# Kernel optimization log

Measured on AMD Instinct MI355X. Metric: run time of the kernel, lower is better.

Reference implementation:

```python
import jax, jax.numpy as jnp
import numpy as np

N, E, F, H, G, C = 50000, 800000, 128, 128, 500, 10
L = 3  # num_conv_layers
EPS = 1e-5


def batch_norm(x, g, b):
    # training-mode BatchNorm1d: biased variance, eps=1e-5
    mu = jnp.mean(x, axis=0)
    var = jnp.var(x, axis=0)
    return (x - mu) * jax.lax.rsqrt(var + EPS) * g + b


def gcn_conv(x, W, bias, src, dst, n):
    # x' = D^{-1/2} (A + I) D^{-1/2} (x W) + bias, edge weights = 1
    xw = x @ W
    loop = jnp.arange(n)
    s = jnp.concatenate([src, loop])  # sources incl. self-loops
    d = jnp.concatenate([dst, loop])  # targets incl. self-loops
    w = jnp.ones(s.shape[0], x.dtype)
    deg = jax.ops.segment_sum(w, s, num_segments=n)
    dinv = jnp.where(deg > 0, jax.lax.rsqrt(deg), 0.0)
    norm = dinv[s] * w * dinv[d]
    msg = xw[s] * norm[:, None]  # gather + scale
    out = jax.ops.segment_sum(msg, d, num_segments=n)  # scatter-add
    return out + bias


def setup_inputs() -> dict:
    key = jax.random.key(0)
    ks = jax.random.split(key, 16)
    x = jax.random.normal(ks[0], (N, F), dtype=jnp.float32)
    edge_index = jax.random.randint(ks[1], (2, E), 0, N, dtype=jnp.int64)
    batch = jnp.sort(jax.random.randint(ks[2], (N,), 0, G, dtype=jnp.int64))
    sF = 1.0 / np.sqrt(F)
    sH = 1.0 / np.sqrt(H)
    return {
        "x": x,
        "edge_index": edge_index,
        "batch": batch,
        "bn_feat_g": jnp.ones((F,), jnp.float32),
        "bn_feat_b": jnp.full((F,), 1e-4, jnp.float32),
        "W_feat": jax.random.normal(ks[3], (F, H), jnp.float32) * sF,
        "bns_conv_g": jnp.ones((L, H), jnp.float32),
        "bns_conv_b": jnp.full((L, H), 1e-4, jnp.float32),
        "W_conv": jax.random.normal(ks[4], (L, H, H), jnp.float32) * sH,
        "b_conv": jnp.zeros((L, H), jnp.float32),
        "bn_fc_g": jnp.ones((H,), jnp.float32),
        "bn_fc_b": jnp.full((H,), 1e-4, jnp.float32),
        "W_lin": jax.random.normal(ks[5], (H, H), jnp.float32) * sH,
        "b_lin": jnp.zeros((H,), jnp.float32),
        "bn_hid_g": jnp.ones((H,), jnp.float32),
        "bn_hid_b": jnp.full((H,), 1e-4, jnp.float32),
        "W_cls": jax.random.normal(ks[6], (H, C), jnp.float32) * sH,
        "b_cls": jnp.zeros((C,), jnp.float32),
    }


def reference(x, edge_index, batch, bn_feat_g, bn_feat_b, W_feat,
              bns_conv_g, bns_conv_b, W_conv, b_conv,
              bn_fc_g, bn_fc_b, W_lin, b_lin,
              bn_hid_g, bn_hid_b, W_cls, b_cls):
    src, dst = edge_index[0], edge_index[1]
    h = batch_norm(x, bn_feat_g, bn_feat_b)
    h = jax.nn.relu(h @ W_feat)  # gfn conv: linear only, no bias/propagation
    for i in range(L):
        h = batch_norm(h, bns_conv_g[i], bns_conv_b[i])
        h = jax.nn.relu(gcn_conv(h, W_conv[i], b_conv[i], src, dst, N))
    h = jax.ops.segment_sum(h, batch, num_segments=G)  # global_add_pool
    h = batch_norm(h, bn_fc_g, bn_fc_b)
    h = jax.nn.relu(h @ W_lin + b_lin)
    h = batch_norm(h, bn_hid_g, bn_hid_b)
    logits = h @ W_cls + b_cls
    return jax.nn.log_softmax(logits, axis=-1)
```

## Files before the change

### kernel.cpp

```cpp
#include <hip/hip_runtime.h>

#define NF 128
#define EPS 1e-5f
#define KELL 64
#define NPART 8
#define KP 16
#define HB 64
#define HRANGE 32768

typedef unsigned short ushort_t;
typedef unsigned int uint_t;

using bf16x8 = __attribute__((ext_vector_type(8))) short;
using f32x4  = __attribute__((ext_vector_type(4))) float;
using f32x2  = __attribute__((ext_vector_type(2))) float;

static __device__ inline ushort_t f2bf(float f) {
    uint_t u = __float_as_uint(f);
    return (ushort_t)((u + 0x7fffu + ((u >> 16) & 1u)) >> 16);
}


__global__ void k_fill_ell(const int* __restrict__ ei, int* __restrict__ dcnt8,
                           ushort_t* __restrict__ colx8, int E, int n) {
    int e = blockIdx.x * 256 + threadIdx.x;
    int p = blockIdx.x & (NPART - 1);
    if (e < E) {
        int s = ei[e], d = ei[E + e];
        int pos = atomicAdd(&dcnt8[p * n + d], 1);
        if (pos < KP) colx8[((size_t)p * n + d) * KP + pos] = (ushort_t)s;
    }
}

__global__ void k_hist(const int* __restrict__ ei, uint_t* __restrict__ partial, int E) {
    __shared__ uint_t h2[HRANGE / 2];
    int b = blockIdx.x, t = threadIdx.x;
#pragma unroll
    for (int p = 0; p < 2; ++p) {
        int base = p * HRANGE;
        for (int w = t; w < HRANGE / 2; w += 256) h2[w] = 0;
        __syncthreads();
        for (int e = b * 256 + t; e < E; e += HB * 256) {
            unsigned u = (unsigned)(ei[e] - base);
            if (u < HRANGE)
                atomicAdd(&h2[u >> 1], 1u << ((u & 1) << 4));
        }
        __syncthreads();
        uint_t* dst = partial + ((size_t)(p * HB + b) << 14);
        for (int w = t; w < HRANGE / 2; w += 256) dst[w] = h2[w];
        __syncthreads();
    }
}

__global__ void k_finish(const int* __restrict__ dcnt8, const uint_t* __restrict__ partial,
                         int* __restrict__ ucnt, float* __restrict__ dinv,
                         const ushort_t* __restrict__ colx8, ushort_t* __restrict__ colx,
                         ushort_t* __restrict__ BbSent, int n) {
    int i = blockIdx.x * 256 + threadIdx.x;
    if (i < n) {
        {
            int p = i >> 15;
            int u = i & (HRANGE - 1);
            int w = u >> 1, sh = (u & 1) << 4;
            const uint_t* base = partial + ((size_t)(p * HB) << 14) + w;
            uint_t sum = 0;
#pragma unroll 8
            for (int b = 0; b < HB; ++b) sum += base[(size_t)b << 14];
            sum = (sum >> sh) & 0xffffu;
            dinv[i] = rsqrtf((float)sum + 1.0f);
        }
        ushort_t* row = colx + (size_t)i * KELL;
        int w = 0;
#pragma unroll
        for (int p = 0; p < NPART; ++p) {
            int c = dcnt8[p * n + i];
            if (c > KP) c = KP;
            const ushort_t* src = colx8 + ((size_t)p * n + i) * KP;
            for (int j = 0; j < c && w < KELL - 1; ++j) row[w++] = src[j];
        }
        ucnt[i] = w;
        row[w] = (ushort_t)i;
        int len = (w + 16) & ~15;
        for (int q = w + 1; q < len; ++q) row[q] = (ushort_t)n;
    }
    if (blockIdx.x == 0 && threadIdx.x < 64)
        ((uint_t*)BbSent)[threadIdx.x] = 0;
}


__global__ void bn_stats(const float* __restrict__ h, float* __restrict__ stats, int n) {
    int j = threadIdx.x & 127;
    int half = threadIdx.x >> 7;
    float s = 0.f, q = 0.f;
    for (int r = blockIdx.x * 2 + half; r < n; r += gridDim.x * 2) {
        float v = h[r * NF + j];
        s += v;
        q += v * v;
    }
    __shared__ float ls[256], lq[256];
    ls[threadIdx.x] = s; lq[threadIdx.x] = q;
    __syncthreads();
    if (threadIdx.x < 128) {
        atomicAdd(&stats[j], ls[threadIdx.x] + ls[threadIdx.x + 128]);
        atomicAdd(&stats[NF + j], lq[threadIdx.x] + lq[threadIdx.x + 128]);
    }
}


__global__ void pack_w4(const float* __restrict__ W0, const float* __restrict__ W123,
                        ushort_t* __restrict__ Wp) {
    int gidx = blockIdx.x * 256 + threadIdx.x;
    int mat = gidx >> 11, idx = gidx & 2047;
    const float* W = (mat == 0) ? W0 : (W123 + (size_t)(mat - 1) * NF * NF);
    int lane = idx & 63, ct = (idx >> 6) & 7, kc = idx >> 9;
    int m = lane & 15, q = lane >> 4;
    ushort_t o[8];
#pragma unroll
    for (int j = 0; j < 8; ++j)
        o[j] = f2bf(W[(kc * 32 + q * 8 + j) * NF + ct * 16 + m]);
    *(uint4*)&Wp[(size_t)gidx * 8] = *(uint4*)o;
}


#define HSTRIDE 136

__launch_bounds__(256)
__global__ void gemm_mfma(const float* __restrict__ Hh, const ushort_t* __restrict__ Wp,
                          const float* __restrict__ stats, const float* __restrict__ gW,
                          const float* __restrict__ bB, float inv_n,
                          const float* __restrict__ bias, const float* __restrict__ rowscale,
                          float* __restrict__ out, ushort_t* __restrict__ outb,
                          int nrows, int relu, int obf) {
    __shared__ ushort_t hs[64 * HSTRIDE];
    __shared__ float acs[256];
    const int tid = threadIdx.x;
    const int rb = blockIdx.x * 64;

    if (tid < 128) {
        float mean = stats[tid] * inv_n;
        float var = stats[NF + tid] * inv_n - mean * mean;
        float rstd = rsqrtf(var + EPS);
        float a = gW[tid] * rstd;
        acs[tid] = a;
        acs[NF + tid] = bB[tid] - mean * a;
    }
    __syncthreads();
    const float4* ac4 = (const float4*)acs;

#pragma unroll
    for (int p = 0; p < 8; ++p) {
        int idx = p * 256 + tid;
        int r = idx >> 5, k4 = idx & 31;
        int gr = rb + r;
        float4 v = (gr < nrows) ? *(const float4*)&Hh[(size_t)gr * NF + k4 * 4]
                                : make_float4(0.f, 0.f, 0.f, 0.f);
        float4 a4 = ac4[k4], c4 = ac4[32 + k4];
        ushort_t o[4];
        o[0] = f2bf(fmaf(v.x, a4.x, c4.x));
        o[1] = f2bf(fmaf(v.y, a4.y, c4.y));
        o[2] = f2bf(fmaf(v.z, a4.z, c4.z));
        o[3] = f2bf(fmaf(v.w, a4.w, c4.w));
        *(uint2*)&hs[r * HSTRIDE + k4 * 4] = *(uint2*)o;
    }
    __syncthreads();

    const int wave = tid >> 6, lane = tid & 63;
    const int m = lane & 15, q = lane >> 4;
    const ushort_t* arow = &hs[(wave * 16 + m) * HSTRIDE];

    f32x4 acc[8];
#pragma unroll
    for (int ct = 0; ct < 8; ++ct) acc[ct] = (f32x4){0.f, 0.f, 0.f, 0.f};

#pragma unroll
    for (int kc = 0; kc < 4; ++kc) {
        bf16x8 af = *(const bf16x8*)&arow[kc * 32 + q * 8];
        const ushort_t* wp = Wp + kc * 4096 + lane * 8;
#pragma unroll
        for (int ct = 0; ct < 8; ++ct) {
            bf16x8 bfr = *(const bf16x8*)&wp[ct * 512];
            acc[ct] = __builtin_amdgcn_mfma_f32_16x16x32_bf16(af, bfr, acc[ct], 0, 0, 0);
        }
    }

#pragma unroll
    for (int r = 0; r < 4; ++r) {
        int grow = rb + wave * 16 + q * 4 + r;
        if (grow < nrows) {
            float rs = (obf && rowscale) ? rowscale[grow] : 1.0f;
#pragma unroll
            for (int ct = 0; ct < 8; ++ct) {
                int col = ct * 16 + m;
                float v = acc[ct][r] + (bias ? bias[col] : 0.f);
                if (relu) v = fmaxf(v, 0.f);
                if (obf) outb[(size_t)grow * NF + col] = f2bf(v * rs);
                else     out[(size_t)grow * NF + col] = v;
            }
        }
    }
}


__launch_bounds__(256)
__global__ void gemm_bn(const float* __restrict__ Hh, const float* __restrict__ W,
                        const float* __restrict__ stats, const float* __restrict__ gW,
                        const float* __restrict__ bB, float inv_n,
                        const float* __restrict__ bias,
                        float* __restrict__ out, int nrows, int relu) {
    __shared__ float hsb[64][133];
    __shared__ float acs[256];
    const int tid = threadIdx.x;
    const int tx = tid & 15;
    const int ty = tid >> 4;
    const int rb = blockIdx.x * 64;

    if (tid < 128) {
        float mean = stats[tid] * inv_n;
        float var = stats[NF + tid] * inv_n - mean * mean;
        float rstd = rsqrtf(var + EPS);
        float a = gW[tid] * rstd;
        acs[tid] = a;
        acs[NF + tid] = bB[tid] - mean * a;
    }
    __syncthreads();

#pragma unroll 8
    for (int p = 0; p < 32; ++p) {
        int idx = p * 256 + tid;
        int r = idx >> 7, k = idx & 127;
        int gr = rb + r;
        float v = (gr < nrows) ? Hh[(size_t)gr * NF + k] : 0.f;
        hsb[r][k] = fmaf(v, acs[k], acs[NF + k]);
    }
    __syncthreads();

    float acc[4][8];
#pragma unroll
    for (int i = 0; i < 4; ++i)
#pragma unroll
        for (int j = 0; j < 8; ++j) acc[i][j] = 0.f;

    const int c0 = tx * 4, c1 = 64 + tx * 4;
#pragma unroll 4
    for (int k = 0; k < 128; ++k) {
        const float4 b0 = *(const float4*)&W[k * NF + c0];
        const float4 b1 = *(const float4*)&W[k * NF + c1];
#pragma unroll
        for (int i = 0; i < 4; ++i) {
            float a = hsb[ty * 4 + i][k];
            acc[i][0] = fmaf(a, b0.x, acc[i][0]);
            acc[i][1] = fmaf(a, b0.y, acc[i][1]);
            acc[i][2] = fmaf(a, b0.z, acc[i][2]);
            acc[i][3] = fmaf(a, b0.w, acc[i][3]);
            acc[i][4] = fmaf(a, b1.x, acc[i][4]);
            acc[i][5] = fmaf(a, b1.y, acc[i][5]);
            acc[i][6] = fmaf(a, b1.z, acc[i][6]);
            acc[i][7] = fmaf(a, b1.w, acc[i][7]);
        }
    }

#pragma unroll
    for (int i = 0; i < 4; ++i) {
        int gr = rb + ty * 4 + i;
        if (gr < nrows) {
            float o[8];
#pragma unroll
            for (int j = 0; j < 8; ++j) {
                int c = (j < 4) ? (c0 + j) : (c1 + j - 4);
                float v = acc[i][j] + (bias ? bias[c] : 0.f);
                o[j] = relu ? fmaxf(v, 0.f) : v;
            }
            *(float4*)&out[(size_t)gr * NF + c0] = make_float4(o[0], o[1], o[2], o[3]);
            *(float4*)&out[(size_t)gr * NF + c1] = make_float4(o[4], o[5], o[6], o[7]);
        }
    }
}


#define ACC2(u, j) { f32x2 t;                                   \
    t.x = __uint_as_float((u) << 16);                           \
    t.y = __uint_as_float((u) & 0xffff0000u);                   \
    acc2[j] += t; }
#define ACC8(q) { ACC2(q.x, 0) ACC2(q.y, 1) ACC2(q.z, 2) ACC2(q.w, 3) }

__launch_bounds__(256)
__global__ void k_aggregate_bf(const ushort_t* __restrict__ xwb, const int* __restrict__ ucnt,
                               const ushort_t* __restrict__ colx, const float* __restrict__ dinv,
                               const float* __restrict__ bias, float* __restrict__ out, int n) {
    int node = blockIdx.x * 16 + (threadIdx.x >> 4);
    int lane = threadIdx.x & 15;
    if (node >= n) return;
    const uint4* __restrict__ xq = (const uint4*)xwb;
    f32x2 acc2[4];
#pragma unroll
    for (int j = 0; j < 4; ++j) acc2[j] = (f32x2){0.f, 0.f};
    int dc = min(ucnt[node], KELL - 1);
    int len = (dc + 16) & ~15;
    int e0 = node * KELL;
    for (int e = e0; e < e0 + len; e += 16) {
        uint4 ia = *(const uint4*)&colx[e];
        uint4 ib = *(const uint4*)&colx[e + 8];
        int i0 = ia.x & 0xffff, i1 = ia.x >> 16;
        int i2 = ia.y & 0xffff, i3 = ia.y >> 16;
        int i4 = ia.z & 0xffff, i5 = ia.z >> 16;
        int i6 = ia.w & 0xffff, i7 = ia.w >> 16;
        int i8 = ib.x & 0xffff, i9 = ib.x >> 16;
        int iA = ib.y & 0xffff, iB = ib.y >> 16;
        int iC = ib.z & 0xffff, iD = ib.z >> 16;
        int iE = ib.w & 0xffff, iF = ib.w >> 16;
        uint4 q0 = xq[(size_t)i0 * 16 + lane];
        uint4 q1 = xq[(size_t)i1 * 16 + lane];
        uint4 q2 = xq[(size_t)i2 * 16 + lane];
        uint4 q3 = xq[(size_t)i3 * 16 + lane];
        uint4 q4 = xq[(size_t)i4 * 16 + lane];
        uint4 q5 = xq[(size_t)i5 * 16 + lane];
        uint4 q6 = xq[(size_t)i6 * 16 + lane];
        uint4 q7 = xq[(size_t)i7 * 16 + lane];
        uint4 q8 = xq[(size_t)i8 * 16 + lane];
        uint4 q9 = xq[(size_t)i9 * 16 + lane];
        uint4 qA = xq[(size_t)iA * 16 + lane];
        uint4 qB = xq[(size_t)iB * 16 + lane];
        uint4 qC = xq[(size_t)iC * 16 + lane];
        uint4 qD = xq[(size_t)iD * 16 + lane];
        uint4 qE = xq[(size_t)iE * 16 + lane];
        uint4 qF = xq[(size_t)iF * 16 + lane];
        ACC8(q0) ACC8(q1) ACC8(q2) ACC8(q3)
        ACC8(q4) ACC8(q5) ACC8(q6) ACC8(q7)
        ACC8(q8) ACC8(q9) ACC8(qA) ACC8(qB)
        ACC8(qC) ACC8(qD) ACC8(qE) ACC8(qF)
    }
    float di = dinv[node];
    float4 b0 = *(const float4*)&bias[lane * 8];
    float4 b1 = *(const float4*)&bias[lane * 8 + 4];
    float4 o0, o1;
    o0.x = fmaxf(fmaf(di, acc2[0].x, b0.x), 0.f);
    o0.y = fmaxf(fmaf(di, acc2[0].y, b0.y), 0.f);
    o0.z = fmaxf(fmaf(di, acc2[1].x, b0.z), 0.f);
    o0.w = fmaxf(fmaf(di, acc2[1].y, b0.w), 0.f);
    o1.x = fmaxf(fmaf(di, acc2[2].x, b1.x), 0.f);
    o1.y = fmaxf(fmaf(di, acc2[2].y, b1.y), 0.f);
    o1.z = fmaxf(fmaf(di, acc2[3].x, b1.z), 0.f);
    o1.w = fmaxf(fmaf(di, acc2[3].y, b1.w), 0.f);
    *(float4*)&out[(size_t)node * NF + lane * 8] = o0;
    *(float4*)&out[(size_t)node * NF + lane * 8 + 4] = o1;
}


__global__ void k_pool(const float* __restrict__ h, const int* __restrict__ batch,
                       float* __restrict__ pooled, float* __restrict__ stats, int n) {
    int g = blockIdx.x;
    int t = threadIdx.x;
    int lo = 0, hi = n;
    while (lo < hi) { int m = (lo + hi) >> 1; if (batch[m] < g) lo = m + 1; else hi = m; }
    int start = lo;
    lo = start; hi = n;
    while (lo < hi) { int m = (lo + hi) >> 1; if (batch[m] < g + 1) lo = m + 1; else hi = m; }
    int end = lo;
    float a0 = 0.f, a1 = 0.f, a2 = 0.f, a3 = 0.f;
    int r = start;
    for (; r + 4 <= end; r += 4) {
        a0 += h[(size_t)r * NF + t];
        a1 += h[(size_t)(r + 1) * NF + t];
        a2 += h[(size_t)(r + 2) * NF + t];
        a3 += h[(size_t)(r + 3) * NF + t];
    }
    for (; r < end; ++r) a0 += h[(size_t)r * NF + t];
    float val = (a0 + a1) + (a2 + a3);
    pooled[g * NF + t] = val;
    atomicAdd(&stats[t], val);
    atomicAdd(&stats[NF + t], val * val);
}


__global__ void k_cls(const float* __restrict__ h, const float* __restrict__ stats,
                      const float* __restrict__ gW, const float* __restrict__ bB,
                      float inv_n, const float* __restrict__ Wc,
                      const float* __restrict__ bc, float* __restrict__ out, int C_) {
    __shared__ float hr[128];
    __shared__ float lg[16];
    __shared__ float lse_s;
    int r = blockIdx.x, t = threadIdx.x;
#pragma unroll
    for (int half = 0; half < 2; ++half) {
        int j = t + half * 64;
        float mean = stats[j] * inv_n;
        float var = stats[NF + j] * inv_n - mean * mean;
        float rstd = rsqrtf(var + EPS);
        float a = gW[j] * rstd;
        float c = bB[j] - mean * a;
        hr[j] = fmaf(h[r * NF + j], a, c);
    }
    __syncthreads();
    if (t < C_) {
        float s = bc[t];
        for (int k = 0; k < 128; ++k) s = fmaf(hr[k], Wc[k * C_ + t], s);
        lg[t] = s;
    }
    __syncthreads();
    if (t == 0) {
        float m = -1e30f;
        for (int c = 0; c < C_; ++c) m = fmaxf(m, lg[c]);
        float se = 0.f;
        for (int c = 0; c < C_; ++c) se += expf(lg[c] - m);
        lse_s = m + logf(se);
    }
    __syncthreads();
    if (t < C_) out[r * C_ + t] = lg[t] - lse_s;
}


extern "C" void kernel_launch(void* const* d_in, const int* in_sizes, int n_in,
                              void* d_out, int out_size, void* d_ws, size_t ws_size,
                              hipStream_t stream) {
    const float* x          = (const float*)d_in[0];
    const int*   ei         = (const int*)d_in[1];
    const int*   batch      = (const int*)d_in[2];
    const float* bn_feat_g  = (const float*)d_in[3];
    const float* bn_feat_b  = (const float*)d_in[4];
    const float* W_feat     = (const float*)d_in[5];
    const float* bns_conv_g = (const float*)d_in[6];
    const float* bns_conv_b = (const float*)d_in[7];
    const float* W_conv     = (const float*)d_in[8];
    const float* b_conv     = (const float*)d_in[9];
    const float* bn_fc_g    = (const float*)d_in[10];
    const float* bn_fc_b    = (const float*)d_in[11];
    const float* W_lin      = (const float*)d_in[12];
    const float* b_lin      = (const float*)d_in[13];
    const float* bn_hid_g   = (const float*)d_in[14];
    const float* bn_hid_b   = (const float*)d_in[15];
    const float* W_cls      = (const float*)d_in[16];
    const float* b_cls      = (const float*)d_in[17];
    float* outp = (float*)d_out;

    const int N_ = in_sizes[2];
    const int E_ = in_sizes[1] / 2;
    const int C_ = 10;
    const int G_ = out_size / C_;

    char* wsp = (char*)d_ws;
    auto alloc = [&](size_t bytes) {
        void* p = (void*)wsp;
        wsp += (bytes + 255) & ~(size_t)255;
        return p;
    };
    int*      dcnt8  = (int*)alloc((size_t)NPART * N_ * 4);
    float*    statsA = (float*)alloc(6 * 256 * 4);
    float*    A      = (float*)alloc((size_t)N_ * NF * 4);
    ushort_t* Bb     = (ushort_t*)alloc((size_t)(N_ + 1) * NF * 2);
    float*    dinv   = (float*)alloc((size_t)N_ * 4);
    int*      ucnt   = (int*)alloc((size_t)N_ * 4);
    ushort_t* colx8  = (ushort_t*)alloc((size_t)NPART * N_ * KP * 2);
    ushort_t* colx   = (ushort_t*)alloc((size_t)N_ * KELL * 2);
    uint_t*   hpart  = (uint_t*)alloc((size_t)2 * HB * (HRANGE / 2) * 4);
    ushort_t* Wp     = (ushort_t*)alloc((size_t)4 * NF * NF * 2);
    float*    pooled = (float*)alloc((size_t)G_ * NF * 4);
    float*    y2     = (float*)alloc((size_t)G_ * NF * 4);

    float* st_x  = statsA;
    float* st_f  = statsA + 256;
    float* st_a1 = statsA + 512;
    float* st_a2 = statsA + 768;
    float* st_pl = statsA + 1024;
    float* st_y2 = statsA + 1280;

    int nb_n = (N_ + 255) / 256;
    int nb_e = (E_ + 255) / 256;
    int nb_g = (N_ + 63) / 64;

    size_t cnt_rounded = (((size_t)NPART * N_ * 4) + 255) & ~(size_t)255;
    hipMemsetAsync(dcnt8, 0, cnt_rounded + 6 * 256 * 4, stream);

    k_fill_ell<<<nb_e, 256, 0, stream>>>(ei, dcnt8, colx8, E_, N_);
    k_hist<<<HB, 256, 0, stream>>>(ei, hpart, E_);
    k_finish<<<nb_n, 256, 0, stream>>>(dcnt8, hpart, ucnt, dinv, colx8, colx,
                                       Bb + (size_t)N_ * NF, N_);

    pack_w4<<<32, 256, 0, stream>>>(W_feat, W_conv, Wp);

    bn_stats<<<512, 256, 0, stream>>>(x, st_x, N_);
    gemm_mfma<<<nb_g, 256, 0, stream>>>(x, Wp, st_x, bn_feat_g, bn_feat_b, 1.0f / N_,
                                        nullptr, nullptr, A, nullptr, N_, 1, 0);
    bn_stats<<<512, 256, 0, stream>>>(A, st_f, N_);

    float* st_in[3] = {st_f, st_a1, st_a2};
    float* st_out[3] = {st_a1, st_a2, nullptr};
    for (int l = 0; l < 3; ++l) {
        gemm_mfma<<<nb_g, 256, 0, stream>>>(A, Wp + (size_t)(l + 1) * NF * NF,
                                            st_in[l], bns_conv_g + l * NF, bns_conv_b + l * NF,
                                            1.0f / N_, nullptr, dinv, nullptr, Bb, N_, 0, 1);
        k_aggregate_bf<<<(N_ + 15) / 16, 256, 0, stream>>>(Bb, ucnt, colx, dinv,
                                                           b_conv + l * NF, A, N_);
        if (st_out[l])
            bn_stats<<<512, 256, 0, stream>>>(A, st_out[l], N_);
    }

    k_pool<<<G_, 128, 0, stream>>>(A, batch, pooled, st_pl, N_);

    gemm_bn<<<(G_ + 63) / 64, 256, 0, stream>>>(pooled, W_lin, st_pl, bn_fc_g, bn_fc_b,
                                                1.0f / G_, b_lin, y2, G_, 1);
    bn_stats<<<512, 256, 0, stream>>>(y2, st_y2, G_);

    k_cls<<<G_, 64, 0, stream>>>(y2, st_y2, bn_hid_g, bn_hid_b, 1.0f / G_,
                                 W_cls, b_cls, outp, C_);
}
```

Baseline: 503.4 us.

## Build ELL adjacency via two-level bucketing by destination block in LDS

Replaces the per-partition global atomic ELL fill and its later merge with a bucket pass: edges are binned by destination block of 256 nodes using shared-memory counts plus one global atomic per bucket. A second kernel then builds each block's ELL rows in LDS and writes them out coalesced. This removes the large 8-partition count array, its memset and the scattered global atomics. The cost is a fixed bucket capacity (BCAP), so overflow edges are dropped, and a hard limit of 256 buckets, i.e. at most 65536 nodes. The order of neighbours within a row becomes nondeterministic.

```diff
diff --git a/kernel.cpp b/kernel.cpp
--- a/kernel.cpp
+++ b/kernel.cpp
@@ -3,10 +3,9 @@
 #define NF 128
 #define EPS 1e-5f
 #define KELL 64
-#define NPART 8
-#define KP 16
 #define HB 64
 #define HRANGE 32768
+#define BCAP 5120
 
 typedef unsigned short ushort_t;
 typedef unsigned int uint_t;
@@ -21,14 +20,33 @@
 }
 
 
-__global__ void k_fill_ell(const int* __restrict__ ei, int* __restrict__ dcnt8,
-                           ushort_t* __restrict__ colx8, int E, int n) {
-    int e = blockIdx.x * 256 + threadIdx.x;
-    int p = blockIdx.x & (NPART - 1);
-    if (e < E) {
+__launch_bounds__(1024)
+__global__ void k_bucket(const int* __restrict__ ei, uint_t* __restrict__ gcnt,
+                         uint_t* __restrict__ bedge, int E) {
+    __shared__ uint_t cnt[256];
+    __shared__ uint_t cur[256];
+    __shared__ uint_t base[256];
+    const int t = threadIdx.x;
+    if (t < 256) { cnt[t] = 0; cur[t] = 0; }
+    __syncthreads();
+    const int chunk = (E + gridDim.x - 1) / gridDim.x;
+    const int e0 = blockIdx.x * chunk;
+    const int e1 = min(e0 + chunk, E);
+    for (int e = e0 + t; e < e1; e += 1024)
+        atomicAdd(&cnt[ei[E + e] >> 8], 1);
+    __syncthreads();
+    if (t < 256) {
+        uint_t c = cnt[t];
+        base[t] = c ? atomicAdd(&gcnt[t], c) : 0u;
+    }
+    __syncthreads();
+    for (int e = e0 + t; e < e1; e += 1024) {
         int s = ei[e], d = ei[E + e];
-        int pos = atomicAdd(&dcnt8[p * n + d], 1);
-        if (pos < KP) colx8[((size_t)p * n + d) * KP + pos] = (ushort_t)s;
+        int b = d >> 8;
+        uint_t pos = base[b] + atomicAdd(&cur[b], 1);
+        if (pos < BCAP)
+            bedge[((size_t)b << 12) + ((size_t)b << 10) + pos] =
+                ((uint_t)(d & 255) << 16) | (uint_t)s;
     }
 }
 
@@ -52,39 +70,53 @@
     }
 }
 
-__global__ void k_finish(const int* __restrict__ dcnt8, const uint_t* __restrict__ partial,
-                         int* __restrict__ ucnt, float* __restrict__ dinv,
-                         const ushort_t* __restrict__ colx8, ushort_t* __restrict__ colx,
-                         ushort_t* __restrict__ BbSent, int n) {
-    int i = blockIdx.x * 256 + threadIdx.x;
+__launch_bounds__(256)
+__global__ void k_build(const uint_t* __restrict__ gcnt, const uint_t* __restrict__ bedge,
+                        const uint_t* __restrict__ hpart, int* __restrict__ ucnt,
+                        float* __restrict__ dinv, ushort_t* __restrict__ colx,
+                        ushort_t* __restrict__ BbSent, int n) {
+    __shared__ ushort_t ell[256][KELL];
+    __shared__ uint_t lcnt[256];
+    const int b = blockIdx.x, t = threadIdx.x;
+    lcnt[t] = 0;
+    __syncthreads();
+    const int nb = min((int)gcnt[b], BCAP);
+    const int node0 = b << 8;
+    const uint_t* bsrc = bedge + ((size_t)b << 12) + ((size_t)b << 10);
+    for (int e = t; e < nb; e += 256) {
+        uint_t pk = bsrc[e];
+        int dl = (pk >> 16) & 255;
+        uint_t pos = atomicAdd(&lcnt[dl], 1);
+        if (pos < KELL - 1) ell[dl][pos] = (ushort_t)(pk & 0xffffu);
+    }
+    __syncthreads();
+    const int i = node0 + t;
     if (i < n) {
-        {
-            int p = i >> 15;
-            int u = i & (HRANGE - 1);
-            int w = u >> 1, sh = (u & 1) << 4;
-            const uint_t* base = partial + ((size_t)(p * HB) << 14) + w;
-            uint_t sum = 0;
+        int w = min((int)lcnt[t], KELL - 1);
+        ell[t][w] = (ushort_t)i;
+        int len = (w + 16) & ~15;
+        for (int q = w + 1; q < len; ++q) ell[t][q] = (ushort_t)n;
+        ucnt[i] = w;
+        int p = i >> 15;
+        int u = i & (HRANGE - 1);
+        int wd = u >> 1, sh = (u & 1) << 4;
+        const uint_t* basep = hpart + ((size_t)(p * HB) << 14) + wd;
+        uint_t sum = 0;
 #pragma unroll 8
-            for (int b = 0; b < HB; ++b) sum += base[(size_t)b << 14];
-            sum = (sum >> sh) & 0xffffu;
-            dinv[i] = rsqrtf((float)sum + 1.0f);
-        }
-        ushort_t* row = colx + (size_t)i * KELL;
-        int w = 0;
-#pragma unroll
-        for (int p = 0; p < NPART; ++p) {
-            int c = dcnt8[p * n + i];
-            if (c > KP) c = KP;
-            const ushort_t* src = colx8 + ((size_t)p * n + i) * KP;
-            for (int j = 0; j < c && w < KELL - 1; ++j) row[w++] = src[j];
-        }
-        ucnt[i] = w;
-        row[w] = (ushort_t)i;
-        int len = (w + 16) & ~15;
-        for (int q = w + 1; q < len; ++q) row[q] = (ushort_t)n;
-    }
-    if (blockIdx.x == 0 && threadIdx.x < 64)
-        ((uint_t*)BbSent)[threadIdx.x] = 0;
+        for (int bb = 0; bb < HB; ++bb) sum += basep[(size_t)bb << 14];
+        sum = (sum >> sh) & 0xffffu;
+        dinv[i] = rsqrtf((float)sum + 1.0f);
+    }
+    __syncthreads();
+    int nrow = min(n - node0, 256);
+    if (nrow > 0) {
+        const uint4* src = (const uint4*)&ell[0][0];
+        uint4* dst = (uint4*)&colx[(size_t)node0 * KELL];
+        int lim = nrow * (KELL * 2 / 16);
+        for (int wds = t; wds < lim; wds += 256) dst[wds] = src[wds];
+    }
+    if (b == 0 && t < 64)
+        ((uint_t*)BbSent)[t] = 0;
 }
 
 
@@ -436,6 +468,7 @@
     const int E_ = in_sizes[1] / 2;
     const int C_ = 10;
     const int G_ = out_size / C_;
+    const int NBUCK = (N_ + 255) >> 8;
 
     char* wsp = (char*)d_ws;
     auto alloc = [&](size_t bytes) {
@@ -443,13 +476,13 @@
         wsp += (bytes + 255) & ~(size_t)255;
         return p;
     };
-    int*      dcnt8  = (int*)alloc((size_t)NPART * N_ * 4);
+    uint_t*   gcnt   = (uint_t*)alloc(256 * 4);
     float*    statsA = (float*)alloc(6 * 256 * 4);
     float*    A      = (float*)alloc((size_t)N_ * NF * 4);
     ushort_t* Bb     = (ushort_t*)alloc((size_t)(N_ + 1) * NF * 2);
     float*    dinv   = (float*)alloc((size_t)N_ * 4);
     int*      ucnt   = (int*)alloc((size_t)N_ * 4);
-    ushort_t* colx8  = (ushort_t*)alloc((size_t)NPART * N_ * KP * 2);
+    uint_t*   bedge  = (uint_t*)alloc((size_t)256 * BCAP * 4);
     ushort_t* colx   = (ushort_t*)alloc((size_t)N_ * KELL * 2);
     uint_t*   hpart  = (uint_t*)alloc((size_t)2 * HB * (HRANGE / 2) * 4);
     ushort_t* Wp     = (ushort_t*)alloc((size_t)4 * NF * NF * 2);
@@ -463,16 +496,13 @@
     float* st_pl = statsA + 1024;
     float* st_y2 = statsA + 1280;
 
-    int nb_n = (N_ + 255) / 256;
-    int nb_e = (E_ + 255) / 256;
     int nb_g = (N_ + 63) / 64;
 
-    size_t cnt_rounded = (((size_t)NPART * N_ * 4) + 255) & ~(size_t)255;
-    hipMemsetAsync(dcnt8, 0, cnt_rounded + 6 * 256 * 4, stream);
-
-    k_fill_ell<<<nb_e, 256, 0, stream>>>(ei, dcnt8, colx8, E_, N_);
+    hipMemsetAsync(gcnt, 0, 1024 + 6 * 256 * 4, stream);
+
+    k_bucket<<<256, 1024, 0, stream>>>(ei, gcnt, bedge, E_);
     k_hist<<<HB, 256, 0, stream>>>(ei, hpart, E_);
-    k_finish<<<nb_n, 256, 0, stream>>>(dcnt8, hpart, ucnt, dinv, colx8, colx,
+    k_build<<<NBUCK, 256, 0, stream>>>(gcnt, bedge, hpart, ucnt, dinv, colx,
                                        Bb + (size_t)N_ * NF, N_);
 
     pack_w4<<<32, 256, 0, stream>>>(W_feat, W_conv, Wp);
```

Measured after the change: 479.3 us. 1.05x faster.
